# Optimization experiments

Measured on AMD Instinct MI355X. Metric: run time of the kernel, lower is better.

The kernel has to match this reference:

```python
import jax, jax.numpy as jnp
import numpy as np


def setup_inputs() -> dict:
    key = jax.random.key(0)
    ks = jax.random.split(key, 8)
    d, h = 1024, 256
    bl, bh = 2048, 2048
    b = bl + bh
    w = lambda k, shp: jax.random.normal(k, shp, jnp.float32) * 0.02
    return {
        "z_low": jax.random.normal(ks[0], (bl, d), jnp.float32),
        "z_high": jax.random.normal(ks[1], (bh, d), jnp.float32),
        "z_bar": jax.random.normal(ks[2], (b, d), jnp.float32),
        "z_normal": jax.random.normal(ks[3], (b, d), jnp.float32),
        "Wa1": w(ks[4], (d, h)), "ba1": jnp.zeros((h,), jnp.float32),
        "Wa2": w(ks[5], (h,)), "ba2": jnp.zeros((), jnp.float32),
        "W0": w(ks[6], (d, d)), "b0": jnp.zeros((d,), jnp.float32),
        "W1": w(ks[7], (d, d)), "b1": jnp.zeros((d,), jnp.float32),
    }


def _scores(x, Wa1, ba1, Wa2, ba2):
    # Linear -> tanh -> Linear(->1); returns per-row attention logits [N]
    return jnp.tanh(x @ Wa1 + ba1) @ Wa2 + ba2


def _integrate(x, Wa1, ba1, Wa2, ba2):
    a = jax.nn.softmax(_scores(x, Wa1, ba1, Wa2, ba2))  # [N]
    return a @ x  # [dim]


def _loo_pool(x, Wa1, ba1, Wa2, ba2):
    # batched leave-one-out attention pooling: row i pools over all j != i
    n = x.shape[0]
    s = _scores(x, Wa1, ba1, Wa2, ba2)  # [N]
    S = jnp.broadcast_to(s[None, :], (n, n))
    S = jnp.where(jnp.eye(n, dtype=bool), -jnp.inf, S)
    A = jax.nn.softmax(S, axis=-1)  # [N,N], zero on diagonal
    return A @ x  # [N, dim]


def _cos(a, b, eps=1e-8):
    na = jnp.maximum(jnp.linalg.norm(a, axis=-1), eps)
    nb = jnp.maximum(jnp.linalg.norm(b, axis=-1), eps)
    return jnp.sum(a * b, axis=-1) / (na * nb)


def reference(z_low, z_high, z_bar, z_normal, Wa1, ba1, Wa2, ba2, W0, b0, W1, b1):
    z_all = jnp.concatenate([z_low, z_high], axis=0)  # [B, d]
    batch = z_all.shape[0]

    z_hat = jnp.concatenate([
        _loo_pool(z_low, Wa1, ba1, Wa2, ba2),
        _loo_pool(z_high, Wa1, ba1, Wa2, ba2),
    ], axis=0)  # [B, d]
    z_tumor = _loo_pool(z_all, Wa1, ba1, Wa2, ba2)  # [B, d]
    z_norm = _integrate(z_normal, Wa1, ba1, Wa2, ba2)  # [d]

    lin0 = lambda v: v @ W0 + b0
    lin1 = lambda v: v @ W1 + b1

    base = lin0(z_hat) + lin1(z_bar)
    pred_tumor = base + lin0(z_tumor)          # [B, d]
    pred_normal = base + lin0(z_norm)[None, :]  # [B, d]

    cpc_tumor = z_all @ pred_tumor.T    # [B, B]
    cpc_normal = z_all @ pred_normal.T  # [B, B]
    eye = jnp.eye(batch, dtype=cpc_tumor.dtype)
    total = eye * cpc_tumor + (1.0 - eye) * cpc_normal

    loss_tcl = jnp.sum(jnp.diag(jax.nn.log_softmax(total, axis=1))) / (-1.0 * batch)

    ones = jnp.ones((batch,), z_all.dtype)
    cos_loss = jnp.mean(ones - _cos(z_all, z_hat)) + jnp.mean(ones - _cos(z_all, z_bar))
    hinge_in = _cos(z_all, pred_tumor) - _cos(z_all, pred_normal)
    hinge = jnp.mean(jnp.maximum(0.0, 1.0 - hinge_in))  # HingeEmbeddingLoss, target=-1, margin=1
    loss_adc = cos_loss + hinge

    return (loss_tcl, loss_adc)
```

## Files before the change

kernel.cpp:

```cpp
#include <hip/hip_runtime.h>
#include <math.h>

#define D     1024
#define H     256
#define BLOW  2048
#define BTOT  4096
#define NCHUNK 64

using bf16x8 = __attribute__((ext_vector_type(8))) __bf16;
using f32x4  = __attribute__((ext_vector_type(4))) float;

static const size_t OFF_ZALL = 0;
static const size_t OFF_C    = 4194304;
static const size_t OFF_PT   = 8388608;
static const size_t T0       = 12582912;
static const size_t OFF_SALL = T0;
static const size_t OFF_SNORM= T0 + 4096;
static const size_t OFF_EGRP = T0 + 8192;
static const size_t OFF_ENORM= T0 + 16384;
static const size_t OFF_PLOW = T0 + 20480;
static const size_t OFF_PHIGH= T0 + 21504;
static const size_t OFF_PNORM= T0 + 22528;
static const size_t OFF_PALL = T0 + 23552;
static const size_t OFF_ZNV  = T0 + 24576;
static const size_t OFF_WNORM= T0 + 25600;
static const size_t OFF_BIASC= T0 + 26624;
static const size_t OFF_STATS= T0 + 27648;
static const size_t OFF_ACC  = T0 + 27664;
static const size_t OFF_NZ   = T0 + 27680;
static const size_t OFF_DT   = T0 + 31776;
static const size_t OFF_G    = T0 + 35872;
static const size_t OFF_DIAG = T0 + 39968;
static const size_t OFF_PART = T0 + 44064;
static const size_t BF_BASE_F = 13160448;
static const size_t BF_ZALLN= 0;
static const size_t BF_ZHAT = 8388608;
static const size_t BF_ZTUM = 12582912;
static const size_t BF_ZBAR = 16777216;
static const size_t BF_C    = 20971520;
static const size_t BF_W0T  = 25165824;
static const size_t BF_W1T  = 26214400;
static const size_t BF_WA1T = 27262976;

__device__ inline unsigned short f2bf(float f){
  unsigned u = __float_as_uint(f);
  u += 0x7fffu + ((u >> 16) & 1u);
  return (unsigned short)(u >> 16);
}
__device__ inline float wave_sum(float v){
#pragma unroll
  for (int o = 32; o > 0; o >>= 1) v += __shfl_xor(v, o);
  return v;
}
__device__ inline float wave_maxf(float v){
#pragma unroll
  for (int o = 32; o > 0; o >>= 1) v = fmaxf(v, __shfl_xor(v, o));
  return v;
}
__device__ inline float block_sum(float v, float* sb){
  v = wave_sum(v);
  __syncthreads();
  if ((threadIdx.x & 63) == 0) sb[threadIdx.x >> 6] = v;
  __syncthreads();
  return sb[0] + sb[1] + sb[2] + sb[3];
}
__device__ inline float block_maxf(float v, float* sb){
  v = wave_maxf(v);
  __syncthreads();
  if ((threadIdx.x & 63) == 0) sb[threadIdx.x >> 6] = v;
  __syncthreads();
  return fmaxf(fmaxf(sb[0], sb[1]), fmaxf(sb[2], sb[3]));
}

__device__ inline void gload16(const unsigned short* g, unsigned short* l){
  __builtin_amdgcn_global_load_lds(
      (const __attribute__((address_space(1))) unsigned int*)g,
      (__attribute__((address_space(3))) unsigned int*)l, 16, 0, 0);
}

__global__ __launch_bounds__(256) void k_prep(const float* __restrict__ zl,
        const float* __restrict__ zh, const float* __restrict__ znorm,
        const float* __restrict__ zbar, float* __restrict__ za,
        unsigned short* __restrict__ zalln_bf, unsigned short* __restrict__ zbar_bf){
  int row = blockIdx.x, t = threadIdx.x, job = blockIdx.z;
  if (job == 0){
    const float4* src = (const float4*)((row < BLOW) ? (zl + (size_t)row * D)
                                                     : (zh + (size_t)(row - BLOW) * D));
    float4 v = src[t];
    ((float4*)(za + (size_t)row * D))[t] = v;
    *(ushort4*)(zalln_bf + (size_t)row * D + t * 4) =
        make_ushort4(f2bf(v.x), f2bf(v.y), f2bf(v.z), f2bf(v.w));
  } else if (job == 1){
    float4 v = ((const float4*)(znorm + (size_t)row * D))[t];
    *(ushort4*)(zalln_bf + (size_t)(BTOT + row) * D + t * 4) =
        make_ushort4(f2bf(v.x), f2bf(v.y), f2bf(v.z), f2bf(v.w));
  } else {
    float4 v = ((const float4*)(zbar + (size_t)row * D))[t];
    *(ushort4*)(zbar_bf + (size_t)row * D + t * 4) =
        make_ushort4(f2bf(v.x), f2bf(v.y), f2bf(v.z), f2bf(v.w));
  }
}

__global__ __launch_bounds__(256) void k_tconv3(const float* __restrict__ W0,
        const float* __restrict__ W1, const float* __restrict__ Wa1,
        unsigned short* __restrict__ W0T, unsigned short* __restrict__ W1T,
        unsigned short* __restrict__ Wa1T){
  __shared__ float tile[32][33];
  int z = blockIdx.z;
  const float* in; unsigned short* out; int R, C;
  if (z == 0){ in = W0; out = W0T; R = D; C = D; }
  else if (z == 1){ in = W1; out = W1T; R = D; C = D; }
  else { if (blockIdx.x >= 8) return; in = Wa1; out = Wa1T; R = D; C = H; }
  int t = threadIdx.x;
  int lr = t >> 3;
  int lc = (t & 7) << 2;
  int gr = blockIdx.y * 32, gc = blockIdx.x * 32;
  float4 v = *(const float4*)(in + (size_t)(gr + lr) * C + gc + lc);
  tile[lr][lc + 0] = v.x; tile[lr][lc + 1] = v.y; tile[lr][lc + 2] = v.z; tile[lr][lc + 3] = v.w;
  __syncthreads();
  ushort4 o = make_ushort4(f2bf(tile[lc + 0][lr]), f2bf(tile[lc + 1][lr]),
                           f2bf(tile[lc + 2][lr]), f2bf(tile[lc + 3][lr]));
  *(ushort4*)(out + (size_t)(gc + lr) * R + gr + lc) = o;
}

__global__ __launch_bounds__(256) void k_zero13(float* __restrict__ ws){
  int i = blockIdx.x * 256 + threadIdx.x;
  if (i < 8192) ws[OFF_SALL + i] = 0.f;
  else if (i < 12288) ws[OFF_PLOW + i - 8192] = 0.f;
  else if (i < 13312) ws[OFF_WNORM + i - 12288] = 0.f;
  else if (i < 13328) ws[OFF_ACC + i - 13312] = 0.f;
}

__device__ inline void mfma_core97(const unsigned short* __restrict__ A,
                                   const unsigned short* __restrict__ B,
                                   int row0, int col0,
                                   unsigned short* As, unsigned short* Bs,
                                   f32x4 acc[4][4]){
  int t = threadIdx.x;
  int l = t & 63, w = t >> 6;
  int wrow = w >> 1, wcol = w & 1;
  int g = l >> 4, c15 = l & 15;
  const unsigned short* a0 = A + (size_t)(row0 + (t >> 2)) * 1024 + ((t & 3) << 3);
  const unsigned short* a1 = a0 + (size_t)64 * 1024;
  const unsigned short* b0 = B + (size_t)(col0 + (t >> 2)) * 1024 + ((t & 3) << 3);
  const unsigned short* b1 = b0 + (size_t)64 * 1024;
  unsigned short* asd  = As + (size_t)w * 512;
  unsigned short* asd1 = asd + 2048;
  unsigned short* bsd  = Bs + (size_t)w * 512;
  unsigned short* bsd1 = bsd + 2048;
  int abase = (wrow * 64 + c15) * 32 + g * 8;
  int bbase = (wcol * 64 + c15) * 32 + g * 8;
  for (int kb = 0; kb < 1024; kb += 32){
    gload16(a0 + kb, asd);
    gload16(a1 + kb, asd1);
    gload16(b0 + kb, bsd);
    gload16(b1 + kb, bsd1);
    __syncthreads();
    bf16x8 af[4], bfr[4];
#pragma unroll
    for (int m = 0; m < 4; ++m) af[m]  = *(const bf16x8*)&As[abase + m * 512];
#pragma unroll
    for (int n = 0; n < 4; ++n) bfr[n] = *(const bf16x8*)&Bs[bbase + n * 512];
#pragma unroll
    for (int m = 0; m < 4; ++m)
#pragma unroll
      for (int n = 0; n < 4; ++n)
        acc[m][n] = __builtin_amdgcn_mfma_f32_16x16x32_bf16(af[m], bfr[n], acc[m][n], 0, 0, 0);
    __syncthreads();
  }
}

__global__ __launch_bounds__(256) void k_scores_bf(const unsigned short* __restrict__ Zbf,
        const unsigned short* __restrict__ Wa1T, const float* __restrict__ ba1,
        const float* __restrict__ Wa2, float* __restrict__ S){
  __shared__ __align__(16) unsigned short smem[8192];
  f32x4 acc[4][4];
  f32x4 zz = {0.f, 0.f, 0.f, 0.f};
#pragma unroll
  for (int m = 0; m < 4; ++m)
#pragma unroll
    for (int n = 0; n < 4; ++n) acc[m][n] = zz;
  int row0 = blockIdx.y * 128, col0 = blockIdx.x * 128;
  mfma_core97(Zbf, Wa1T, row0, col0, smem, smem + 4096, acc);
  int t = threadIdx.x, l = t & 63, w = t >> 6, wrow = w >> 1, wcol = w & 1;
  int g = l >> 4, c15 = l & 15;
#pragma unroll
  for (int m = 0; m < 4; ++m){
#pragma unroll
    for (int r = 0; r < 4; ++r){
      float v = 0.f;
#pragma unroll
      for (int n = 0; n < 4; ++n){
        int col = col0 + wcol * 64 + n * 16 + c15;
        float x = acc[m][n][r] + ba1[col];
        float e = __expf(2.f * x);
        v += (1.f - 2.f / (e + 1.f)) * Wa2[col];
      }
      v += __shfl_xor(v, 1); v += __shfl_xor(v, 2); v += __shfl_xor(v, 4); v += __shfl_xor(v, 8);
      if (c15 == 0) atomicAdd(&S[row0 + wrow * 64 + m * 16 + 4 * g + r], v);
    }
  }
}

__global__ __launch_bounds__(256) void k_gemm_bf(const unsigned short* __restrict__ A,
        const unsigned short* __restrict__ B, const unsigned short* __restrict__ A2,
        const unsigned short* __restrict__ B2, const float* __restrict__ Add,
        const float* __restrict__ bias, float* __restrict__ Out,
        unsigned short* __restrict__ OutBf){
  __shared__ __align__(16) unsigned short smem[8192];
  f32x4 acc[4][4];
  f32x4 zz = {0.f, 0.f, 0.f, 0.f};
#pragma unroll
  for (int m = 0; m < 4; ++m)
#pragma unroll
    for (int n = 0; n < 4; ++n) acc[m][n] = zz;
  int row0 = blockIdx.y * 128, col0 = blockIdx.x * 128;
  mfma_core97(A, B, row0, col0, smem, smem + 4096, acc);
  if (A2) mfma_core97(A2, B2, row0, col0, smem, smem + 4096, acc);
  int t = threadIdx.x, l = t & 63, w = t >> 6, wrow = w >> 1, wcol = w & 1;
  int g = l >> 4, c15 = l & 15;
#pragma unroll
  for (int m = 0; m < 4; ++m){
    int row = row0 + wrow * 64 + m * 16 + 4 * g;
#pragma unroll
    for (int n = 0; n < 4; ++n){
      int col = col0 + wcol * 64 + n * 16 + c15;
#pragma unroll
      for (int r = 0; r < 4; ++r){
        float v = acc[m][n][r];
        size_t idx = (size_t)(row + r) * 1024 + col;
        if (Add)  v += Add[idx];
        if (bias) v += bias[col];
        Out[idx] = v;
        if (OutBf) OutBf[idx] = f2bf(v);
      }
    }
  }
}

__global__ __launch_bounds__(256) void k_gemm_lse(const unsigned short* __restrict__ A,
        const unsigned short* __restrict__ B, float2* __restrict__ partials,
        float* __restrict__ diagM){
  __shared__ __align__(16) unsigned short smem[8192];
  f32x4 acc[4][4];
  f32x4 zz = {0.f, 0.f, 0.f, 0.f};
#pragma unroll
  for (int m = 0; m < 4; ++m)
#pragma unroll
    for (int n = 0; n < 4; ++n) acc[m][n] = zz;
  int row0 = blockIdx.y * 128, col0 = blockIdx.x * 128;
  mfma_core97(A, B, row0, col0, smem, smem + 4096, acc);
  int t = threadIdx.x, l = t & 63, w = t >> 6, wrow = w >> 1, wcol = w & 1;
  int g = l >> 4, c15 = l & 15;
  int chunk = blockIdx.x * 2 + wcol;
#pragma unroll
  for (int m = 0; m < 4; ++m){
#pragma unroll
    for (int r = 0; r < 4; ++r){
      float lm = acc[m][0][r];
#pragma unroll
      for (int n = 1; n < 4; ++n) lm = fmaxf(lm, acc[m][n][r]);
      lm = fmaxf(lm, __shfl_xor(lm, 1));
      lm = fmaxf(lm, __shfl_xor(lm, 2));
      lm = fmaxf(lm, __shfl_xor(lm, 4));
      lm = fmaxf(lm, __shfl_xor(lm, 8));
      float ls = 0.f;
#pragma unroll
      for (int n = 0; n < 4; ++n) ls += __expf(acc[m][n][r] - lm);
      ls += __shfl_xor(ls, 1); ls += __shfl_xor(ls, 2); ls += __shfl_xor(ls, 4); ls += __shfl_xor(ls, 8);
      if (c15 == 0)
        partials[(size_t)chunk * BTOT + (row0 + wrow * 64 + m * 16 + 4 * g + r)] = make_float2(lm, ls);
    }
  }
  if (blockIdx.x == blockIdx.y && wrow == wcol && ((c15 >> 2) == g)){
#pragma unroll
    for (int m = 0; m < 4; ++m)
      diagM[row0 + wrow * 64 + m * 16 + c15] = acc[m][m][c15 & 3];
  }
}

__global__ __launch_bounds__(256) void k_stats(const float* __restrict__ s_all,
        const float* __restrict__ s_norm, float* __restrict__ e_grp,
        float* __restrict__ e_norm, float* __restrict__ stats){
  __shared__ float sb[4];
  int t = threadIdx.x;
  float va[16], vn[16];
#pragma unroll
  for (int j = 0; j < 16; ++j) va[j] = s_all[t + 256 * j];
#pragma unroll
  for (int j = 0; j < 16; ++j) vn[j] = s_norm[t + 256 * j];
  float m = -1e30f;
#pragma unroll
  for (int j = 0; j < 8; ++j) m = fmaxf(m, va[j]);
  float ml = block_maxf(m, sb);
  m = -1e30f;
#pragma unroll
  for (int j = 8; j < 16; ++j) m = fmaxf(m, va[j]);
  float mh = block_maxf(m, sb);
  m = -1e30f;
#pragma unroll
  for (int j = 0; j < 16; ++j) m = fmaxf(m, vn[j]);
  float mn = block_maxf(m, sb);
  float ma = fmaxf(ml, mh);
  float a = 0.f;
#pragma unroll
  for (int j = 0; j < 8; ++j){ float e = __expf(va[j] - ml); e_grp[t + 256 * j] = e; a += e; }
  float tl = block_sum(a, sb);
  a = 0.f;
#pragma unroll
  for (int j = 8; j < 16; ++j){ float e = __expf(va[j] - mh); e_grp[t + 256 * j] = e; a += e; }
  float th = block_sum(a, sb);
  a = 0.f;
#pragma unroll
  for (int j = 0; j < 16; ++j){ float e = __expf(vn[j] - mn); e_norm[t + 256 * j] = e; a += e; }
  float tn = block_sum(a, sb);
  if (t == 0){
    float sl = __expf(ml - ma), sh = __expf(mh - ma);
    stats[0] = ml; stats[1] = tl; stats[2] = mh; stats[3] = th;
    stats[4] = ma; stats[5] = tl * sl + th * sh; stats[6] = mn; stats[7] = tn;
    stats[8] = sl; stats[9] = sh;
  }
}

__global__ __launch_bounds__(256) void k_pvec(const float* __restrict__ z_all,
        const float* __restrict__ z_normal, const float* __restrict__ e_grp,
        const float* __restrict__ e_norm, float* __restrict__ P){
  int gz = blockIdx.z;
  const float* X; const float* E; float* Pg; int nr;
  if (gz == 0){ X = z_all;                         E = e_grp;        Pg = P;        nr = BLOW; }
  else if (gz == 1){ X = z_all + (size_t)BLOW * D; E = e_grp + BLOW; Pg = P + 1024; nr = BLOW; }
  else { X = z_normal;                             E = e_norm;       Pg = P + 2048; nr = BTOT; }
  int r0 = blockIdx.y * 16;
  if (r0 >= nr) return;
  int c4 = threadIdx.x * 4;
  float4 a = make_float4(0.f, 0.f, 0.f, 0.f);
#pragma unroll 4
  for (int r = r0; r < r0 + 16; ++r){
    float e = E[r];
    float4 x = *(const float4*)(X + (size_t)r * D + c4);
    a.x = fmaf(e, x.x, a.x); a.y = fmaf(e, x.y, a.y);
    a.z = fmaf(e, x.z, a.z); a.w = fmaf(e, x.w, a.w);
  }
  atomicAdd(&Pg[c4 + 0], a.x);
  atomicAdd(&Pg[c4 + 1], a.y);
  atomicAdd(&Pg[c4 + 2], a.z);
  atomicAdd(&Pg[c4 + 3], a.w);
}

__global__ __launch_bounds__(256) void k_smallvec(const float* __restrict__ P,
        const float* __restrict__ stats, const float* __restrict__ b0,
        const float* __restrict__ b1, float* __restrict__ P_all,
        float* __restrict__ znv, float* __restrict__ biasC){
  int c = blockIdx.x * 256 + threadIdx.x;
  znv[c] = P[2048 + c] / stats[7];
  biasC[c] = 2.f * b0[c] + b1[c];
  P_all[c] = stats[8] * P[c] + stats[9] * P[1024 + c];
}

__global__ __launch_bounds__(256) void k_wnorm(const float* __restrict__ znv,
        const float* __restrict__ W0, float* __restrict__ w_norm){
  int col = blockIdx.x * 256 + threadIdx.x;
  int kc = blockIdx.y;
  float a = 0.f;
  for (int k = kc * 128; k < kc * 128 + 128; ++k)
    a = fmaf(znv[k], W0[(size_t)k * D + col], a);
  atomicAdd(&w_norm[col], a);
}

__global__ __launch_bounds__(256) void k_zhat(const float* __restrict__ z_all,
        const float* __restrict__ z_bar, const float* __restrict__ e_grp,
        const float* __restrict__ stats,
        const float* __restrict__ P_low, const float* __restrict__ P_high,
        const float* __restrict__ P_all, unsigned short* __restrict__ zhat_bf,
        unsigned short* __restrict__ ztum_bf, float* __restrict__ nz_arr,
        float* __restrict__ accum){
  __shared__ float sb[4];
  int i = blockIdx.x, t = threadIdx.x;
  const float* Pg = (i < BLOW) ? P_low : P_high;
  float Tg = (i < BLOW) ? stats[1] : stats[3];
  float Ta = stats[5];
  float eg = e_grp[i];
  float ea = eg * ((i < BLOW) ? stats[8] : stats[9]);
  float ig = 1.f / (Tg - eg), ia = 1.f / (Ta - ea);
  size_t base = (size_t)i * D;
  float4 x  = ((const float4*)(z_all + base))[t];
  float4 pg = ((const float4*)Pg)[t];
  float4 pa = ((const float4*)P_all)[t];
  float4 zb = ((const float4*)(z_bar + base))[t];
  float4 zh, zt;
  zh.x = (pg.x - eg * x.x) * ig; zh.y = (pg.y - eg * x.y) * ig;
  zh.z = (pg.z - eg * x.z) * ig; zh.w = (pg.w - eg * x.w) * ig;
  zt.x = (pa.x - ea * x.x) * ia; zt.y = (pa.y - ea * x.y) * ia;
  zt.z = (pa.z - ea * x.z) * ia; zt.w = (pa.w - ea * x.w) * ia;
  *(ushort4*)(zhat_bf + base + t * 4) = make_ushort4(f2bf(zh.x), f2bf(zh.y), f2bf(zh.z), f2bf(zh.w));
  *(ushort4*)(ztum_bf + base + t * 4) = make_ushort4(f2bf(zt.x), f2bf(zt.y), f2bf(zt.z), f2bf(zt.w));
  float nz2 = x.x*x.x + x.y*x.y + x.z*x.z + x.w*x.w;
  float nh2 = zh.x*zh.x + zh.y*zh.y + zh.z*zh.z + zh.w*zh.w;
  float dzh = x.x*zh.x + x.y*zh.y + x.z*zh.z + x.w*zh.w;
  float nb2 = zb.x*zb.x + zb.y*zb.y + zb.z*zb.z + zb.w*zb.w;
  float dzb = x.x*zb.x + x.y*zb.y + x.z*zb.z + x.w*zb.w;
  float s_nz2 = block_sum(nz2, sb);
  float s_nh2 = block_sum(nh2, sb);
  float s_dzh = block_sum(dzh, sb);
  float s_nb2 = block_sum(nb2, sb);
  float s_dzb = block_sum(dzb, sb);
  if (t == 0){
    float nz = sqrtf(s_nz2);
    nz_arr[i] = nz;
    float denA = fmaxf(nz, 1e-8f) * fmaxf(sqrtf(s_nh2), 1e-8f);
    float denB = fmaxf(nz, 1e-8f) * fmaxf(sqrtf(s_nb2), 1e-8f);
    atomicAdd(&accum[0], (1.f - s_dzh / denA) + (1.f - s_dzb / denB));
  }
}

__global__ __launch_bounds__(256) void k_rowred2(const float* __restrict__ z_all,
        const float* __restrict__ PT, const float* __restrict__ C,
        const float* __restrict__ w_norm, const float* __restrict__ nz_arr,
        float* __restrict__ dt_arr, float* __restrict__ g_arr, float* __restrict__ accum){
  __shared__ float sb[4];
  int i = blockIdx.x, t = threadIdx.x;
  size_t base = (size_t)i * D;
  float4 x  = ((const float4*)(z_all + base))[t];
  float4 pt = ((const float4*)(PT + base))[t];
  float4 c  = ((const float4*)(C + base))[t];
  float4 wv = ((const float4*)w_norm)[t];
  float4 pn = make_float4(c.x + wv.x, c.y + wv.y, c.z + wv.z, c.w + wv.w);
  float dt   = x.x*pt.x + x.y*pt.y + x.z*pt.z + x.w*pt.w;
  float npt2 = pt.x*pt.x + pt.y*pt.y + pt.z*pt.z + pt.w*pt.w;
  float dpn  = x.x*pn.x + x.y*pn.y + x.z*pn.z + x.w*pn.w;
  float npn2 = pn.x*pn.x + pn.y*pn.y + pn.z*pn.z + pn.w*pn.w;
  float gg   = x.x*wv.x + x.y*wv.y + x.z*wv.z + x.w*wv.w;
  float s_dt   = block_sum(dt, sb);
  float s_npt2 = block_sum(npt2, sb);
  float s_dpn  = block_sum(dpn, sb);
  float s_npn2 = block_sum(npn2, sb);
  float s_g    = block_sum(gg, sb);
  if (t == 0){
    dt_arr[i] = s_dt; g_arr[i] = s_g;
    float nz = fmaxf(nz_arr[i], 1e-8f);
    float ct = s_dt  / (nz * fmaxf(sqrtf(s_npt2), 1e-8f));
    float cn = s_dpn / (nz * fmaxf(sqrtf(s_npn2), 1e-8f));
    atomicAdd(&accum[1], fmaxf(0.f, 1.f - (ct - cn)));
  }
}

__global__ __launch_bounds__(256) void k_combine(const float2* __restrict__ partials,
        const float* __restrict__ diagM, const float* __restrict__ dt,
        const float* __restrict__ g, float* __restrict__ accum){
  __shared__ float sb[4];
  int i = blockIdx.x * 256 + threadIdx.x;
  float m = -1e30f, S = 0.f;
  for (int c = 0; c < NCHUNK; ++c){
    float2 p = partials[(size_t)c * BTOT + i];
    float nm = fmaxf(m, p.x);
    S = S * __expf(m - nm) + p.y * __expf(p.x - nm);
    m = nm;
  }
  float vold = diagM[i];
  float vnew = dt[i] - g[i];
  float nm = fmaxf(m, vnew);
  float S2 = S * __expf(m - nm) - __expf(vold - nm) + __expf(vnew - nm);
  float lse = g[i] + nm + logf(S2);
  float contrib = lse - dt[i];
  float tot = block_sum(contrib, sb);
  if (threadIdx.x == 0) atomicAdd(&accum[2], tot);
}

__global__ void k_final(const float* __restrict__ accum, float* __restrict__ out){
  out[0] = accum[2] / (float)BTOT;
  out[1] = (accum[0] + accum[1]) / (float)BTOT;
}

extern "C" void kernel_launch(void* const* d_in, const int* in_sizes, int n_in,
                              void* d_out, int out_size, void* d_ws, size_t ws_size,
                              hipStream_t stream){
  const float* z_low    = (const float*)d_in[0];
  const float* z_high   = (const float*)d_in[1];
  const float* z_bar    = (const float*)d_in[2];
  const float* z_normal = (const float*)d_in[3];
  const float* Wa1      = (const float*)d_in[4];
  const float* ba1      = (const float*)d_in[5];
  const float* Wa2      = (const float*)d_in[6];
  const float* ba2      = (const float*)d_in[7];
  const float* W0       = (const float*)d_in[8];
  const float* b0       = (const float*)d_in[9];
  const float* W1       = (const float*)d_in[10];
  const float* b1       = (const float*)d_in[11];
  float* ws = (float*)d_ws;
  unsigned short* bw = (unsigned short*)(ws + BF_BASE_F);
  float* out = (float*)d_out;
  (void)ba2;

  k_prep<<<dim3(BTOT, 1, 3), dim3(256), 0, stream>>>(z_low, z_high, z_normal, z_bar,
      ws + OFF_ZALL, bw + BF_ZALLN, bw + BF_ZBAR);
  k_tconv3<<<dim3(32, 32, 3), dim3(256), 0, stream>>>(W0, W1, Wa1,
      bw + BF_W0T, bw + BF_W1T, bw + BF_WA1T);
  k_zero13<<<dim3(53), dim3(256), 0, stream>>>(ws);

  k_scores_bf<<<dim3(2, 64), dim3(256), 0, stream>>>(bw + BF_ZALLN, bw + BF_WA1T,
      ba1, Wa2, ws + OFF_SALL);

  k_stats<<<dim3(1), dim3(256), 0, stream>>>(ws + OFF_SALL, ws + OFF_SNORM,
      ws + OFF_EGRP, ws + OFF_ENORM, ws + OFF_STATS);

  k_pvec<<<dim3(1, 256, 3), dim3(256), 0, stream>>>(ws + OFF_ZALL, z_normal,
      ws + OFF_EGRP, ws + OFF_ENORM, ws + OFF_PLOW);

  k_smallvec<<<dim3(4), dim3(256), 0, stream>>>(ws + OFF_PLOW, ws + OFF_STATS,
      b0, b1, ws + OFF_PALL, ws + OFF_ZNV, ws + OFF_BIASC);

  k_wnorm<<<dim3(4, 8), dim3(256), 0, stream>>>(ws + OFF_ZNV, W0, ws + OFF_WNORM);

  k_zhat<<<dim3(BTOT), dim3(256), 0, stream>>>(ws + OFF_ZALL, z_bar,
      ws + OFF_EGRP, ws + OFF_STATS,
      ws + OFF_PLOW, ws + OFF_PHIGH, ws + OFF_PALL,
      bw + BF_ZHAT, bw + BF_ZTUM, ws + OFF_NZ, ws + OFF_ACC);

  k_gemm_bf<<<dim3(8, 32), dim3(256), 0, stream>>>(bw + BF_ZHAT, bw + BF_W0T,
      bw + BF_ZBAR, bw + BF_W1T, nullptr, ws + OFF_BIASC, ws + OFF_C, bw + BF_C);
  k_gemm_bf<<<dim3(8, 32), dim3(256), 0, stream>>>(bw + BF_ZTUM, bw + BF_W0T,
      nullptr, nullptr, ws + OFF_C, nullptr, ws + OFF_PT, nullptr);

  k_rowred2<<<dim3(BTOT), dim3(256), 0, stream>>>(ws + OFF_ZALL, ws + OFF_PT,
      ws + OFF_C, ws + OFF_WNORM, ws + OFF_NZ, ws + OFF_DT, ws + OFF_G, ws + OFF_ACC);

  k_gemm_lse<<<dim3(32, 32), dim3(256), 0, stream>>>(bw + BF_ZALLN, bw + BF_C,
      (float2*)(ws + OFF_PART), ws + OFF_DIAG);

  k_combine<<<dim3(16), dim3(256), 0, stream>>>((const float2*)(ws + OFF_PART),
      ws + OFF_DIAG, ws + OFF_DT, ws + OFF_G, ws + OFF_ACC);

  k_final<<<dim3(1), dim3(1), 0, stream>>>(ws + OFF_ACC, out);
}
```

Measured before the change: 455.1 us.

## Double-buffer LDS in MFMA GEMM core and fuse C/PT GEMMs

The shared MFMA k-loop now uses two LDS buffers, so the next K-slice is loaded while the current one is computed, with one barrier per iteration instead of two. The two projection GEMM launches become one kernel. It computes C = Zhat·W0 + Zbar·W1 + bias, stores it, then keeps accumulating Ztum·W0 in the same registers to produce PT without re-reading C from memory. LDS per block doubles to 32 KB, which may lower occupancy.

```diff
diff --git a/kernel.cpp b/kernel.cpp
--- a/kernel.cpp
+++ b/kernel.cpp
@@ -131,11 +131,11 @@
   else if (i < 13328) ws[OFF_ACC + i - 13312] = 0.f;
 }
 
-__device__ inline void mfma_core97(const unsigned short* __restrict__ A,
-                                   const unsigned short* __restrict__ B,
-                                   int row0, int col0,
-                                   unsigned short* As, unsigned short* Bs,
-                                   f32x4 acc[4][4]){
+__device__ inline void mfma_core_db(const unsigned short* __restrict__ A,
+                                    const unsigned short* __restrict__ B,
+                                    int row0, int col0,
+                                    unsigned short* lds,
+                                    f32x4 acc[4][4]){
   int t = threadIdx.x;
   int l = t & 63, w = t >> 6;
   int wrow = w >> 1, wcol = w & 1;
@@ -144,36 +144,42 @@
   const unsigned short* a1 = a0 + (size_t)64 * 1024;
   const unsigned short* b0 = B + (size_t)(col0 + (t >> 2)) * 1024 + ((t & 3) << 3);
   const unsigned short* b1 = b0 + (size_t)64 * 1024;
-  unsigned short* asd  = As + (size_t)w * 512;
-  unsigned short* asd1 = asd + 2048;
-  unsigned short* bsd  = Bs + (size_t)w * 512;
-  unsigned short* bsd1 = bsd + 2048;
+  int sd = w * 512;
   int abase = (wrow * 64 + c15) * 32 + g * 8;
-  int bbase = (wcol * 64 + c15) * 32 + g * 8;
+  int bbase = 4096 + (wcol * 64 + c15) * 32 + g * 8;
+  unsigned short* buf = lds;
+  unsigned short* nxt = lds + 8192;
+  gload16(a0, buf + sd);
+  gload16(a1, buf + 2048 + sd);
+  gload16(b0, buf + 4096 + sd);
+  gload16(b1, buf + 6144 + sd);
+  __syncthreads();
   for (int kb = 0; kb < 1024; kb += 32){
-    gload16(a0 + kb, asd);
-    gload16(a1 + kb, asd1);
-    gload16(b0 + kb, bsd);
-    gload16(b1 + kb, bsd1);
-    __syncthreads();
+    if (kb + 32 < 1024){
+      gload16(a0 + kb + 32, nxt + sd);
+      gload16(a1 + kb + 32, nxt + 2048 + sd);
+      gload16(b0 + kb + 32, nxt + 4096 + sd);
+      gload16(b1 + kb + 32, nxt + 6144 + sd);
+    }
     bf16x8 af[4], bfr[4];
 #pragma unroll
-    for (int m = 0; m < 4; ++m) af[m]  = *(const bf16x8*)&As[abase + m * 512];
-#pragma unroll
-    for (int n = 0; n < 4; ++n) bfr[n] = *(const bf16x8*)&Bs[bbase + n * 512];
+    for (int m = 0; m < 4; ++m) af[m]  = *(const bf16x8*)&buf[abase + m * 512];
+#pragma unroll
+    for (int n = 0; n < 4; ++n) bfr[n] = *(const bf16x8*)&buf[bbase + n * 512];
 #pragma unroll
     for (int m = 0; m < 4; ++m)
 #pragma unroll
       for (int n = 0; n < 4; ++n)
         acc[m][n] = __builtin_amdgcn_mfma_f32_16x16x32_bf16(af[m], bfr[n], acc[m][n], 0, 0, 0);
     __syncthreads();
+    unsigned short* tmp = buf; buf = nxt; nxt = tmp;
   }
 }
 
 __global__ __launch_bounds__(256) void k_scores_bf(const unsigned short* __restrict__ Zbf,
         const unsigned short* __restrict__ Wa1T, const float* __restrict__ ba1,
         const float* __restrict__ Wa2, float* __restrict__ S){
-  __shared__ __align__(16) unsigned short smem[8192];
+  __shared__ __align__(16) unsigned short smem[16384];
   f32x4 acc[4][4];
   f32x4 zz = {0.f, 0.f, 0.f, 0.f};
 #pragma unroll
@@ -181,7 +187,7 @@
 #pragma unroll
     for (int n = 0; n < 4; ++n) acc[m][n] = zz;
   int row0 = blockIdx.y * 128, col0 = blockIdx.x * 128;
-  mfma_core97(Zbf, Wa1T, row0, col0, smem, smem + 4096, acc);
+  mfma_core_db(Zbf, Wa1T, row0, col0, smem, acc);
   int t = threadIdx.x, l = t & 63, w = t >> 6, wrow = w >> 1, wcol = w & 1;
   int g = l >> 4, c15 = l & 15;
 #pragma unroll
@@ -202,12 +208,12 @@
   }
 }
 
-__global__ __launch_bounds__(256) void k_gemm_bf(const unsigned short* __restrict__ A,
-        const unsigned short* __restrict__ B, const unsigned short* __restrict__ A2,
-        const unsigned short* __restrict__ B2, const float* __restrict__ Add,
-        const float* __restrict__ bias, float* __restrict__ Out,
-        unsigned short* __restrict__ OutBf){
-  __shared__ __align__(16) unsigned short smem[8192];
+__global__ __launch_bounds__(256) void k_gemm_cpt(const unsigned short* __restrict__ Zhat,
+        const unsigned short* __restrict__ Zbar, const unsigned short* __restrict__ Ztum,
+        const unsigned short* __restrict__ W0T, const unsigned short* __restrict__ W1T,
+        const float* __restrict__ biasC, float* __restrict__ C,
+        unsigned short* __restrict__ Cbf, float* __restrict__ PT){
+  __shared__ __align__(16) unsigned short smem[16384];
   f32x4 acc[4][4];
   f32x4 zz = {0.f, 0.f, 0.f, 0.f};
 #pragma unroll
@@ -215,8 +221,8 @@
 #pragma unroll
     for (int n = 0; n < 4; ++n) acc[m][n] = zz;
   int row0 = blockIdx.y * 128, col0 = blockIdx.x * 128;
-  mfma_core97(A, B, row0, col0, smem, smem + 4096, acc);
-  if (A2) mfma_core97(A2, B2, row0, col0, smem, smem + 4096, acc);
+  mfma_core_db(Zhat, W0T, row0, col0, smem, acc);
+  mfma_core_db(Zbar, W1T, row0, col0, smem, acc);
   int t = threadIdx.x, l = t & 63, w = t >> 6, wrow = w >> 1, wcol = w & 1;
   int g = l >> 4, c15 = l & 15;
 #pragma unroll
@@ -225,14 +231,28 @@
 #pragma unroll
     for (int n = 0; n < 4; ++n){
       int col = col0 + wcol * 64 + n * 16 + c15;
+      float bv = biasC[col];
 #pragma unroll
       for (int r = 0; r < 4; ++r){
-        float v = acc[m][n][r];
+        float v = acc[m][n][r] + bv;
         size_t idx = (size_t)(row + r) * 1024 + col;
-        if (Add)  v += Add[idx];
-        if (bias) v += bias[col];
-        Out[idx] = v;
-        if (OutBf) OutBf[idx] = f2bf(v);
+        C[idx] = v;
+        Cbf[idx] = f2bf(v);
+      }
+    }
+  }
+  mfma_core_db(Ztum, W0T, row0, col0, smem, acc);
+#pragma unroll
+  for (int m = 0; m < 4; ++m){
+    int row = row0 + wrow * 64 + m * 16 + 4 * g;
+#pragma unroll
+    for (int n = 0; n < 4; ++n){
+      int col = col0 + wcol * 64 + n * 16 + c15;
+      float bv = biasC[col];
+#pragma unroll
+      for (int r = 0; r < 4; ++r){
+        size_t idx = (size_t)(row + r) * 1024 + col;
+        PT[idx] = acc[m][n][r] + bv;
       }
     }
   }
@@ -241,7 +261,7 @@
 __global__ __launch_bounds__(256) void k_gemm_lse(const unsigned short* __restrict__ A,
         const unsigned short* __restrict__ B, float2* __restrict__ partials,
         float* __restrict__ diagM){
-  __shared__ __align__(16) unsigned short smem[8192];
+  __shared__ __align__(16) unsigned short smem[16384];
   f32x4 acc[4][4];
   f32x4 zz = {0.f, 0.f, 0.f, 0.f};
 #pragma unroll
@@ -249,7 +269,7 @@
 #pragma unroll
     for (int n = 0; n < 4; ++n) acc[m][n] = zz;
   int row0 = blockIdx.y * 128, col0 = blockIdx.x * 128;
-  mfma_core97(A, B, row0, col0, smem, smem + 4096, acc);
+  mfma_core_db(A, B, row0, col0, smem, acc);
   int t = threadIdx.x, l = t & 63, w = t >> 6, wrow = w >> 1, wcol = w & 1;
   int g = l >> 4, c15 = l & 15;
   int chunk = blockIdx.x * 2 + wcol;
@@ -516,10 +536,9 @@
       ws + OFF_PLOW, ws + OFF_PHIGH, ws + OFF_PALL,
       bw + BF_ZHAT, bw + BF_ZTUM, ws + OFF_NZ, ws + OFF_ACC);
 
-  k_gemm_bf<<<dim3(8, 32), dim3(256), 0, stream>>>(bw + BF_ZHAT, bw + BF_W0T,
-      bw + BF_ZBAR, bw + BF_W1T, nullptr, ws + OFF_BIASC, ws + OFF_C, bw + BF_C);
-  k_gemm_bf<<<dim3(8, 32), dim3(256), 0, stream>>>(bw + BF_ZTUM, bw + BF_W0T,
-      nullptr, nullptr, ws + OFF_C, nullptr, ws + OFF_PT, nullptr);
+  k_gemm_cpt<<<dim3(8, 32), dim3(256), 0, stream>>>(bw + BF_ZHAT, bw + BF_ZBAR,
+      bw + BF_ZTUM, bw + BF_W0T, bw + BF_W1T, ws + OFF_BIASC,
+      ws + OFF_C, bw + BF_C, ws + OFF_PT);
 
   k_rowred2<<<dim3(BTOT), dim3(256), 0, stream>>>(ws + OFF_ZALL, ws + OFF_PT,
       ws + OFF_C, ws + OFF_WNORM, ws + OFF_NZ, ws + OFF_DT, ws + OFF_G, ws + OFF_ACC);
```

New measurement: 409.3 us. -10.1%, faster.
